# Performance work log

Hardware: AMD Instinct MI355X
Metric: run time of the kernel (lower is better)

## Reference

```python
import jax, jax.numpy as jnp
import numpy as np

D_MODEL, D_STATE, EXPAND = 256, 16, 2
D_INNER = EXPAND * D_MODEL
DT_RANK = (D_MODEL + 15) // 16
BATCH, SEQLEN = 4, 4096


def silu(x):
    return x * jax.nn.sigmoid(x)


def setup_inputs() -> dict:
    key = jax.random.key(0)
    ks = jax.random.split(key, 10)
    h = jax.random.normal(ks[0], (BATCH, SEQLEN, D_MODEL), dtype=jnp.float32)
    Wi_f = jax.random.normal(ks[1], (2 * D_INNER, D_MODEL), dtype=jnp.float32) / np.sqrt(D_MODEL)
    Wi_b = jax.random.normal(ks[2], (2 * D_INNER, D_MODEL), dtype=jnp.float32) / np.sqrt(D_MODEL)
    Wx_f = jax.random.normal(ks[3], (DT_RANK + 2 * D_STATE, D_INNER), dtype=jnp.float32) / np.sqrt(D_INNER)
    Wx_b = jax.random.normal(ks[4], (DT_RANK + 2 * D_STATE, D_INNER), dtype=jnp.float32) / np.sqrt(D_INNER)
    dt_std = DT_RANK ** -0.5
    Wdt_f = jax.random.uniform(ks[5], (D_INNER, DT_RANK), dtype=jnp.float32, minval=-dt_std, maxval=dt_std)
    Wdt_b = jax.random.uniform(ks[6], (D_INNER, DT_RANK), dtype=jnp.float32, minval=-dt_std, maxval=dt_std)
    # dt bias = inverse-softplus of dt sampled log-uniform in [1e-3, 1e-1]
    dt = jnp.exp(jax.random.uniform(ks[7], (D_INNER,), dtype=jnp.float32) * (np.log(0.1) - np.log(0.001)) + np.log(0.001))
    dt = jnp.clip(dt, 1e-4, None)
    inv_dt = dt + jnp.log(-jnp.expm1(-dt))
    bdt_f = inv_dt
    bdt_b = inv_dt
    A_log = jnp.log(jnp.broadcast_to(jnp.arange(1, D_STATE + 1, dtype=jnp.float32), (D_INNER, D_STATE)))
    A_log_f = A_log
    A_log_b = A_log
    D_f = jnp.ones((D_INNER,), dtype=jnp.float32)
    D_b = jnp.ones((D_INNER,), dtype=jnp.float32)
    Wo = jax.random.normal(ks[8], (D_MODEL, 2 * D_INNER), dtype=jnp.float32) / np.sqrt(2 * D_INNER)
    return {"hidden_states": h, "Wi_f": Wi_f, "Wi_b": Wi_b, "Wx_f": Wx_f, "Wx_b": Wx_b,
            "Wdt_f": Wdt_f, "Wdt_b": Wdt_b, "bdt_f": bdt_f, "bdt_b": bdt_b,
            "A_log_f": A_log_f, "A_log_b": A_log_b, "D_f": D_f, "D_b": D_b, "Wo": Wo}


def mamba_dir(h, Wi, Wx, Wdt, bdt, A_log, Dp, reverse):
    b, l, _ = h.shape
    di, r = Wdt.shape
    n = A_log.shape[1]
    xz = h @ Wi.T                      # [b,l,2*di]
    if reverse:
        xz = xz[:, ::-1]
    x, z = xz[..., :di], xz[..., di:]
    u = silu(x)                        # selective_scan input u
    x_dbl = u @ Wx.T                   # [b,l,r+2n]
    delta = jax.nn.softplus(x_dbl[..., :r] @ Wdt.T + bdt)   # [b,l,di]
    Bm = x_dbl[..., r:r + n]           # [b,l,n]
    Cm = x_dbl[..., r + n:r + 2 * n]   # [b,l,n]
    A = -jnp.exp(A_log)                # [di,n]

    def step(s, inp):
        u_t, d_t, B_t, C_t = inp       # [b,di],[b,di],[b,n],[b,n]
        dA = jnp.exp(d_t[..., None] * A)                         # [b,di,n]
        s = dA * s + (d_t * u_t)[..., None] * B_t[:, None, :]    # [b,di,n]
        y_t = jnp.einsum('bdn,bn->bd', s, C_t)
        return s, y_t

    s0 = jnp.zeros((b, di, n), dtype=u.dtype)
    xs = (jnp.swapaxes(u, 0, 1), jnp.swapaxes(delta, 0, 1),
          jnp.swapaxes(Bm, 0, 1), jnp.swapaxes(Cm, 0, 1))
    _, ys = jax.lax.scan(step, s0, xs)
    y = jnp.swapaxes(ys, 0, 1) + u * Dp          # skip term D*u
    y = y * silu(z)                              # gated output
    if reverse:
        y = y[:, ::-1]
    return y


def reference(hidden_states, Wi_f, Wi_b, Wx_f, Wx_b, Wdt_f, Wdt_b, bdt_f, bdt_b, A_log_f, A_log_b, D_f, D_b, Wo):
    y_f = mamba_dir(hidden_states, Wi_f, Wx_f, Wdt_f, bdt_f, A_log_f, D_f, False)
    y_b = mamba_dir(hidden_states, Wi_b, Wx_b, Wdt_b, bdt_b, A_log_b, D_b, True)
    y = jnp.concatenate([y_f, y_b], axis=-1)     # [b,l,2*di]
    return y @ Wo.T                              # [b,l,d_model]
```

## Files before the change

kernel.cpp:

```cpp
#include <hip/hip_runtime.h>
#include <hip/hip_bf16.h>
#include <cstddef>
#include <cstdint>

#define D_MODELc 256
#define D_STATEc 16
#define D_INNERc 512
#define DT_RANKc 16
#define BATCHc   4
#define SEQLENc  4096
#define NCHUNK   128
#define CHUNK    32

typedef unsigned short u16;
typedef __attribute__((ext_vector_type(8))) short bf16x8;
typedef __attribute__((ext_vector_type(4))) float f32x4;

__device__ __forceinline__ float siluf(float v) { return v / (1.f + __expf(-v)); }

__device__ __forceinline__ u16 bf16_rne(float f) {
    uint32_t u = __float_as_uint(f);
    u += 0x7fffu + ((u >> 16) & 1u);
    return (u16)(u >> 16);
}
__device__ __forceinline__ float bf16_to_f(u16 h) {
    return __uint_as_float(((uint32_t)h) << 16);
}
__device__ __forceinline__ float softplusf(float x) {
    return fmaxf(x, 0.f) + __logf(1.f + __expf(-fabsf(x)));
}

#define GLL16(g, l) __builtin_amdgcn_global_load_lds( \
    (const __attribute__((address_space(1))) uint32_t*)(g), \
    (__attribute__((address_space(3))) uint32_t*)(l), 16, 0, 0)

__global__ __launch_bounds__(256) void split_kernel(const float* __restrict__ in,
                                                    u16* __restrict__ hi,
                                                    u16* __restrict__ lo, int n4) {
    int i = blockIdx.x * 256 + threadIdx.x;
    const int stride = gridDim.x * 256;
    for (; i < n4; i += stride) {
        float4 v = ((const float4*)in)[i];
        u16 h0 = bf16_rne(v.x), h1 = bf16_rne(v.y), h2 = bf16_rne(v.z), h3 = bf16_rne(v.w);
        ushort4 hv; hv.x = h0; hv.y = h1; hv.z = h2; hv.w = h3;
        ushort4 lv;
        lv.x = bf16_rne(v.x - bf16_to_f(h0));
        lv.y = bf16_rne(v.y - bf16_to_f(h1));
        lv.z = bf16_rne(v.z - bf16_to_f(h2));
        lv.w = bf16_rne(v.w - bf16_to_f(h3));
        ((ushort4*)hi)[i] = hv;
        ((ushort4*)lo)[i] = lv;
    }
}

template<int EPI, int NBL2>
__global__ __launch_bounds__(256) void gemm_mfma(
        const u16* __restrict__ Ah, const u16* __restrict__ Al, int lda,
        const u16* __restrict__ Bh, const u16* __restrict__ Bl, int ldb,
        float* __restrict__ out0,
        u16* __restrict__ uh, u16* __restrict__ ul,
        int M, int N, int K) {
    __shared__ u16 lds[2][4][4][128][8];
    const int t    = threadIdx.x;
    const int lane = t & 63;
    const int wid  = t >> 6;
    const int wrow = wid >> 1, wcol = wid & 1;

    const int id  = blockIdx.x;
    const int xcd = id & 7;
    const int j   = id >> 3;
    const int nb  = j & ((1 << NBL2) - 1);
    const int mg  = j >> NBL2;
    const int m0  = (mg * 8 + xcd) * 128;
    const int n0  = nb * 128;

    const int lr  = lane & 15;
    const int kgl = lane >> 4;

    f32x4 acc[4][4] = {};

    auto stage = [&](int buf, int k0) {
        #pragma unroll
        for (int i = 0; i < 8; i++) {
            int c    = i * 256 + t;
            int tile = c >> 9;
            int kg   = (c >> 7) & 3;
            int row  = c & 127;
            const u16* bsrc = (tile == 0) ? Ah : (tile == 1) ? Al : (tile == 2) ? Bh : Bl;
            int r0 = (tile < 2) ? m0 : n0;
            int ld = (tile < 2) ? lda : ldb;
            const u16* g = bsrc + (size_t)(r0 + row) * ld + k0 + kg * 8;
            GLL16(g, ((char*)lds) + (size_t)buf * 32768 + (size_t)c * 16);
        }
    };

    const int NT = K >> 5;
    stage(0, 0);
    __syncthreads();

    for (int kt = 0; kt < NT; ++kt) {
        const int buf = kt & 1;
        if (kt + 1 < NT) stage(buf ^ 1, (kt + 1) * 32);

        bf16x8 afh[4], afl[4];
        #pragma unroll
        for (int mi = 0; mi < 4; mi++) {
            afh[mi] = *(const bf16x8*)&lds[buf][0][kgl][wrow * 64 + mi * 16 + lr][0];
            afl[mi] = *(const bf16x8*)&lds[buf][1][kgl][wrow * 64 + mi * 16 + lr][0];
        }
        #pragma unroll
        for (int ni = 0; ni < 4; ni++) {
            bf16x8 bfh = *(const bf16x8*)&lds[buf][2][kgl][wcol * 64 + ni * 16 + lr][0];
            bf16x8 bfl = *(const bf16x8*)&lds[buf][3][kgl][wcol * 64 + ni * 16 + lr][0];
            #pragma unroll
            for (int mi = 0; mi < 4; mi++) {
                acc[mi][ni] = __builtin_amdgcn_mfma_f32_16x16x32_bf16(afh[mi], bfh, acc[mi][ni], 0, 0, 0);
                acc[mi][ni] = __builtin_amdgcn_mfma_f32_16x16x32_bf16(afh[mi], bfl, acc[mi][ni], 0, 0, 0);
                acc[mi][ni] = __builtin_amdgcn_mfma_f32_16x16x32_bf16(afl[mi], bfh, acc[mi][ni], 0, 0, 0);
            }
        }
        __syncthreads();
    }

    #pragma unroll
    for (int mi = 0; mi < 4; mi++) {
        #pragma unroll
        for (int ni = 0; ni < 4; ni++) {
            #pragma unroll
            for (int r = 0; r < 4; r++) {
                int m = m0 + wrow * 64 + mi * 16 + kgl * 4 + r;
                int n = n0 + wcol * 64 + ni * 16 + lr;
                float v = acc[mi][ni][r];
                if (EPI == 0) {
                    out0[(size_t)m * N + n] = v;
                } else {
                    float s = siluf(v);
                    int dirn = n >> 10;
                    int nn   = n & 1023;
                    size_t dof = (size_t)dirn * (size_t)M * 512;
                    if (nn < 512) {
                        size_t idx = dof + (size_t)m * 512 + nn;
                        u16 sh = bf16_rne(s);
                        uh[idx] = sh;
                        ul[idx] = bf16_rne(s - bf16_to_f(sh));
                    } else {
                        out0[dof + (size_t)m * 512 + (nn - 512)] = s;
                    }
                }
            }
        }
    }
}

__global__ __launch_bounds__(256) void xdbl_mfma(
        const u16* __restrict__ Uh, const u16* __restrict__ Ul,
        const u16* __restrict__ WxH, const u16* __restrict__ WxL,
        float* __restrict__ out) {
    __shared__ u16 lds[2][4][64][8];
    const int t    = threadIdx.x;
    const int lane = t & 63;
    const int wid  = t >> 6;
    const int m0   = blockIdx.x * 64;
    const int dir  = blockIdx.y;
    const int Mp   = gridDim.x * 64;
    const int lr   = lane & 15;
    const int kgl  = lane >> 4;

    const size_t dofU = (size_t)dir * (size_t)Mp * 512;
    const size_t dofW = (size_t)dir * (size_t)48 * 512;
    const u16* Ah = Uh + dofU;
    const u16* Al = Ul + dofU;

    f32x4 acc[3] = {};

    for (int k0 = 0; k0 < 512; k0 += 32) {
        #pragma unroll
        for (int i = 0; i < 2; i++) {
            int c    = i * 256 + t;
            int tile = c >> 8;
            int kg   = (c >> 6) & 3;
            int row  = c & 63;
            const u16* bsrc = tile ? Al : Ah;
            const u16* g = bsrc + (size_t)(m0 + row) * 512 + k0 + kg * 8;
            GLL16(g, ((char*)lds) + (size_t)c * 16);
        }
        __syncthreads();

        bf16x8 afh = *(const bf16x8*)&lds[0][kgl][wid * 16 + lr][0];
        bf16x8 afl = *(const bf16x8*)&lds[1][kgl][wid * 16 + lr][0];
        #pragma unroll
        for (int nf = 0; nf < 3; nf++) {
            const size_t boff = dofW + (size_t)(nf * 16 + lr) * 512 + k0 + kgl * 8;
            bf16x8 bfh = *(const bf16x8*)(WxH + boff);
            bf16x8 bfl = *(const bf16x8*)(WxL + boff);
            acc[nf] = __builtin_amdgcn_mfma_f32_16x16x32_bf16(afh, bfh, acc[nf], 0, 0, 0);
            acc[nf] = __builtin_amdgcn_mfma_f32_16x16x32_bf16(afh, bfl, acc[nf], 0, 0, 0);
            acc[nf] = __builtin_amdgcn_mfma_f32_16x16x32_bf16(afl, bfh, acc[nf], 0, 0, 0);
        }
        __syncthreads();
    }

    float* o = out + (size_t)dir * (size_t)Mp * 48;
    #pragma unroll
    for (int nf = 0; nf < 3; nf++) {
        #pragma unroll
        for (int r = 0; r < 4; r++) {
            int m = m0 + wid * 16 + kgl * 4 + r;
            int n = nf * 16 + lr;
            o[(size_t)m * 48 + n] = acc[nf][r];
        }
    }
}

__global__ __launch_bounds__(256) void scan_phaseA(
        const u16* __restrict__ Uh, const u16* __restrict__ Ul,
        const float* __restrict__ XD,
        const float* __restrict__ Wdt_f, const float* __restrict__ Wdt_b,
        const float* __restrict__ bdt_f, const float* __restrict__ bdt_b,
        const float* __restrict__ AL_f, const float* __restrict__ AL_b,
        float* __restrict__ SDL, float* __restrict__ S) {
    const int c   = blockIdx.x;
    const int d   = blockIdx.y * 256 + threadIdx.x;
    const int z   = blockIdx.z;
    const int dir = z & 1;
    const int b   = z >> 1;
    const int PB  = gridDim.z >> 1;
    const int Mp  = PB * SEQLENc;
    const float* Wdt = dir ? Wdt_b : Wdt_f;
    const float* bdt = dir ? bdt_b : bdt_f;
    const float* AL  = dir ? AL_b  : AL_f;
    const u16* UhD = Uh + (size_t)dir * Mp * 512;
    const u16* UlD = Ul + (size_t)dir * Mp * 512;
    const float* XDD = XD + (size_t)dir * Mp * 48;

    float w[16], a[16], s[16];
    #pragma unroll
    for (int n = 0; n < 16; n++) {
        w[n] = Wdt[d * 16 + n];
        a[n] = -__expf(AL[d * 16 + n]);
        s[n] = 0.f;
    }
    const float a0 = a[0];
    bool pw = (a0 != 0.f);
    #pragma unroll
    for (int n = 1; n < 16; n++)
        pw = pw && (fabsf(a[n] - (float)(n + 1) * a0) <= 3e-6f * fabsf(a[n]));
    const float bb = bdt[d];
    float sdl = 0.f;

    for (int i = 0; i < CHUNK; i++) {
        int tt = c * CHUNK + i;
        int l  = dir ? (SEQLENc - 1 - tt) : tt;
        size_t row = (size_t)b * SEQLENc + l;
        float uu = bf16_to_f(UhD[row * 512 + d]) + bf16_to_f(UlD[row * 512 + d]);
        const float4* xr4 = (const float4*)&XDD[row * 48];
        float acc = bb;
        #pragma unroll
        for (int k = 0; k < 4; k++) {
            float4 xa = xr4[k];
            acc += xa.x*w[k*4+0] + xa.y*w[k*4+1] + xa.z*w[k*4+2] + xa.w*w[k*4+3];
        }
        float dl = softplusf(acc);
        sdl += dl;
        float du = dl * uu;
        if (pw) {
            float q = __expf(a0 * dl);
            float dAn = 1.f;
            #pragma unroll
            for (int g = 0; g < 4; g++) {
                float4 B4 = xr4[4 + g];
                float bx[4] = {B4.x, B4.y, B4.z, B4.w};
                #pragma unroll
                for (int jj = 0; jj < 4; jj++) {
                    int n = g * 4 + jj;
                    dAn *= q;
                    s[n] = dAn * s[n] + du * bx[jj];
                }
            }
        } else {
            #pragma unroll
            for (int g = 0; g < 4; g++) {
                float4 B4 = xr4[4 + g];
                float bx[4] = {B4.x, B4.y, B4.z, B4.w};
                #pragma unroll
                for (int jj = 0; jj < 4; jj++) {
                    int n = g * 4 + jj;
                    float dA = __expf(dl * a[n]);
                    s[n] = dA * s[n] + du * bx[jj];
                }
            }
        }
    }
    SDL[((size_t)z * NCHUNK + c) * 512 + d] = sdl;
    size_t base = (((size_t)z * NCHUNK + c) * 16) * 512 + d;
    #pragma unroll
    for (int n = 0; n < 16; n++)
        S[base + (size_t)n * 512] = s[n];
}

__global__ __launch_bounds__(256) void scan_phaseB(const float* __restrict__ SDL,
                                                   float* __restrict__ S,
                                                   const float* __restrict__ AL_f,
                                                   const float* __restrict__ AL_b) {
    const int g   = blockIdx.x * 256 + threadIdx.x;
    const int d   = g & 511;
    const int n   = (g >> 9) & 15;
    const int z   = g >> 13;
    const int dir = z & 1;
    const float an = -__expf((dir ? AL_b : AL_f)[d * 16 + n]);
    const size_t strideS = (size_t)16 * 512;
    size_t offS = (((size_t)z * NCHUNK) * 16 + n) * 512 + d;
    size_t offD = ((size_t)z * NCHUNK) * 512 + d;
    float carry = 0.f;
    float sdl = SDL[offD], ss = S[offS];
    for (int c = 0; c < NCHUNK; c++) {
        float sdn = 0.f, sn = 0.f;
        if (c + 1 < NCHUNK) { sdn = SDL[offD + 512]; sn = S[offS + strideS]; }
        float pp = __expf(an * sdl);
        S[offS] = carry;
        carry = pp * carry + ss;
        sdl = sdn; ss = sn;
        offS += strideS; offD += 512;
    }
}

__global__ __launch_bounds__(256) void scan_phaseC(
        const u16* __restrict__ Uh, const u16* __restrict__ Ul,
        const float* __restrict__ XD,
        const float* __restrict__ Wdt_f, const float* __restrict__ Wdt_b,
        const float* __restrict__ bdt_f, const float* __restrict__ bdt_b,
        const float* __restrict__ AL_f, const float* __restrict__ AL_b,
        const float* __restrict__ E,
        const float* __restrict__ SZ,
        const float* __restrict__ D_f,  const float* __restrict__ D_b,
        u16* __restrict__ Yh, u16* __restrict__ Yl) {
    const int c   = blockIdx.x;
    const int d   = blockIdx.y * 256 + threadIdx.x;
    const int z   = blockIdx.z;
    const int dir = z & 1;
    const int b   = z >> 1;
    const int PB  = gridDim.z >> 1;
    const int Mp  = PB * SEQLENc;
    const float* Wdt = dir ? Wdt_b : Wdt_f;
    const float* bdt = dir ? bdt_b : bdt_f;
    const float* AL  = dir ? AL_b  : AL_f;
    const u16* UhD = Uh + (size_t)dir * Mp * 512;
    const u16* UlD = Ul + (size_t)dir * Mp * 512;
    const float* XDD = XD + (size_t)dir * Mp * 48;
    const float* SZD = SZ + (size_t)dir * Mp * 512;

    float w[16], a[16], s[16];
    size_t base = (((size_t)z * NCHUNK + c) * 16) * 512 + d;
    #pragma unroll
    for (int n = 0; n < 16; n++) {
        w[n] = Wdt[d * 16 + n];
        a[n] = -__expf(AL[d * 16 + n]);
        s[n] = E[base + (size_t)n * 512];
    }
    const float a0 = a[0];
    bool pw = (a0 != 0.f);
    #pragma unroll
    for (int n = 1; n < 16; n++)
        pw = pw && (fabsf(a[n] - (float)(n + 1) * a0) <= 3e-6f * fabsf(a[n]));
    const float bb = bdt[d];
    const float Dd = (dir ? D_b : D_f)[d];

    for (int i = 0; i < CHUNK; i++) {
        int tt = c * CHUNK + i;
        int l  = dir ? (SEQLENc - 1 - tt) : tt;
        size_t row = (size_t)b * SEQLENc + l;
        float uu = bf16_to_f(UhD[row * 512 + d]) + bf16_to_f(UlD[row * 512 + d]);
        const float4* xr4 = (const float4*)&XDD[row * 48];
        float acc = bb;
        #pragma unroll
        for (int k = 0; k < 4; k++) {
            float4 xa = xr4[k];
            acc += xa.x*w[k*4+0] + xa.y*w[k*4+1] + xa.z*w[k*4+2] + xa.w*w[k*4+3];
        }
        float dl = softplusf(acc);
        float du = dl * uu;
        float y = 0.f;
        if (pw) {
            float q = __expf(a0 * dl);
            float dAn = 1.f;
            #pragma unroll
            for (int g = 0; g < 4; g++) {
                float4 B4 = xr4[4 + g];
                float4 C4 = xr4[8 + g];
                float bx[4] = {B4.x, B4.y, B4.z, B4.w};
                float cx[4] = {C4.x, C4.y, C4.z, C4.w};
                #pragma unroll
                for (int jj = 0; jj < 4; jj++) {
                    int n = g * 4 + jj;
                    dAn *= q;
                    s[n] = dAn * s[n] + du * bx[jj];
                    y += s[n] * cx[jj];
                }
            }
        } else {
            #pragma unroll
            for (int g = 0; g < 4; g++) {
                float4 B4 = xr4[4 + g];
                float4 C4 = xr4[8 + g];
                float bx[4] = {B4.x, B4.y, B4.z, B4.w};
                float cx[4] = {C4.x, C4.y, C4.z, C4.w};
                #pragma unroll
                for (int jj = 0; jj < 4; jj++) {
                    int n = g * 4 + jj;
                    float dA = __expf(dl * a[n]);
                    s[n] = dA * s[n] + du * bx[jj];
                    y += s[n] * cx[jj];
                }
            }
        }
        float yv = (y + uu * Dd) * SZD[row * 512 + d];
        size_t yi = row * 1024 + (size_t)dir * 512 + d;
        u16 yh = bf16_rne(yv);
        Yh[yi] = yh;
        Yl[yi] = bf16_rne(yv - bf16_to_f(yh));
    }
}

extern "C" void kernel_launch(void* const* d_in, const int* in_sizes, int n_in,
                              void* d_out, int out_size, void* d_ws, size_t ws_size,
                              hipStream_t stream) {
    const float* h    = (const float*)d_in[0];
    const float* Wi_f = (const float*)d_in[1];
    const float* Wi_b = (const float*)d_in[2];
    const float* Wx_f = (const float*)d_in[3];
    const float* Wx_b = (const float*)d_in[4];
    const float* Wdt_f= (const float*)d_in[5];
    const float* Wdt_b= (const float*)d_in[6];
    const float* bdt_f= (const float*)d_in[7];
    const float* bdt_b= (const float*)d_in[8];
    const float* Al_f = (const float*)d_in[9];
    const float* Al_b = (const float*)d_in[10];
    const float* D_f  = (const float*)d_in[11];
    const float* D_b  = (const float*)d_in[12];
    const float* Wo   = (const float*)d_in[13];
    float* out = (float*)d_out;

    const size_t W_ELE  = 1024 * 256;
    const size_t WX_ELE = 48 * 512;
    const size_t FB   = (size_t)SEQLENc * D_INNERc;
    const size_t FH   = (size_t)SEQLENc * D_MODELc;
    const size_t FX   = (size_t)SEQLENc * 48;
    const size_t FP   = (size_t)NCHUNK * 16 * 512;
    const size_t FD   = (size_t)NCHUNK * 512;
    const size_t FY   = (size_t)SEQLENc * 1024;

    const size_t fixed_bytes = (8 * W_ELE + 4 * WX_ELE) * sizeof(u16);
    const size_t per_b = 2 * FH * sizeof(u16)
                       + 2 * FB * sizeof(float)
                       + 4 * FB * sizeof(u16)
                       + 2 * FX * sizeof(float)
                       + 2 * (FP + FD) * sizeof(float)
                       + 2 * FY * sizeof(u16);
    int PB = 4;
    if (fixed_bytes + 4 * per_b + 65536 > ws_size) PB = 2;
    if (fixed_bytes + 2 * per_b + 65536 > ws_size) PB = 1;

    char* cur = (char*)d_ws;
    auto alloc = [&](size_t bytes) -> char* {
        char* p = cur; cur += (bytes + 255) & ~(size_t)255; return p;
    };
    u16* WiH = (u16*)alloc(2 * W_ELE * 2);
    u16* WiL = (u16*)alloc(2 * W_ELE * 2);
    u16* WoH = (u16*)alloc(W_ELE * 2);
    u16* WoL = (u16*)alloc(W_ELE * 2);
    u16* WxH = (u16*)alloc(2 * WX_ELE * 2);
    u16* WxL = (u16*)alloc(2 * WX_ELE * 2);
    u16*   hH = (u16*)alloc((size_t)PB * FH * 2);
    u16*   hL = (u16*)alloc((size_t)PB * FH * 2);
    float* sz = (float*)alloc((size_t)PB * 2 * FB * 4);
    u16*   uhB= (u16*)alloc((size_t)PB * 2 * FB * 2);
    u16*   ulB= (u16*)alloc((size_t)PB * 2 * FB * 2);
    float* xd = (float*)alloc((size_t)PB * 2 * FX * 4);
    float* SDL= (float*)alloc((size_t)PB * 2 * FD * 4);
    float* S  = (float*)alloc((size_t)PB * 2 * FP * 4);
    u16*   yH = (u16*)alloc((size_t)PB * FY * 2);
    u16*   yL = (u16*)alloc((size_t)PB * FY * 2);

    {
        int n4 = (int)(W_ELE / 4);
        int blocks = (n4 + 255) / 256; if (blocks > 1024) blocks = 1024;
        split_kernel<<<blocks, 256, 0, stream>>>(Wi_f, WiH, WiL, n4);
        split_kernel<<<blocks, 256, 0, stream>>>(Wi_b, WiH + W_ELE, WiL + W_ELE, n4);
        split_kernel<<<blocks, 256, 0, stream>>>(Wo,   WoH, WoL, n4);
        int nx4 = (int)(WX_ELE / 4);
        split_kernel<<<(nx4 + 255) / 256, 256, 0, stream>>>(Wx_f, WxH, WxL, nx4);
        split_kernel<<<(nx4 + 255) / 256, 256, 0, stream>>>(Wx_b, WxH + WX_ELE, WxL + WX_ELE, nx4);
    }

    for (int b0 = 0; b0 < BATCHc; b0 += PB) {
        const int Mp = PB * SEQLENc;
        const int MB = Mp / 128;
        const float* hB = h   + (size_t)b0 * FH;
        float*       oB = out + (size_t)b0 * FH;

        {
            int n4 = (int)((size_t)PB * FH / 4);
            int blocks = (n4 + 255) / 256; if (blocks > 2048) blocks = 2048;
            split_kernel<<<blocks, 256, 0, stream>>>(hB, hH, hL, n4);
        }

        gemm_mfma<1, 4><<<16 * MB, 256, 0, stream>>>(
            hH, hL, D_MODELc, WiH, WiL, D_MODELc,
            sz, uhB, ulB, Mp, 2048, D_MODELc);

        xdbl_mfma<<<dim3(Mp / 64, 2), 256, 0, stream>>>(uhB, ulB, WxH, WxL, xd);

        scan_phaseA<<<dim3(NCHUNK, 2, 2 * PB), 256, 0, stream>>>(
            uhB, ulB, xd, Wdt_f, Wdt_b, bdt_f, bdt_b, Al_f, Al_b, SDL, S);
        scan_phaseB<<<PB * 64, 256, 0, stream>>>(SDL, S, Al_f, Al_b);
        scan_phaseC<<<dim3(NCHUNK, 2, 2 * PB), 256, 0, stream>>>(
            uhB, ulB, xd, Wdt_f, Wdt_b, bdt_f, bdt_b, Al_f, Al_b,
            S, sz, D_f, D_b, yH, yL);

        gemm_mfma<0, 1><<<2 * MB, 256, 0, stream>>>(
            yH, yL, 1024, WoH, WoL, 1024,
            oB, nullptr, nullptr, Mp, D_MODELc, 1024);
    }
}
```

Baseline: 371.6 us.

## Interleave hi/lo bf16 split pairs into packed 32-bit words and use nontemporal accesses

Stores the hi/lo bf16 split of u and y as one packed 32-bit word per element instead of two separate u16 arrays. The scan kernels then read a single 4-byte word per element, and the GEMM and xdbl kernels unpack fragments from LDS with a new interleaved staging path. Most global loads and stores also become nontemporal hints, aiming to cut separate scattered 2-byte transactions and cache pollution. The cost is extra ALU work to unpack fragments, and the nontemporal hints may hurt when data is reused through the cache.

Result: slower. 416.9 us (+12.2%).

```diff
diff --git a/kernel.cpp b/kernel.cpp
--- a/kernel.cpp
+++ b/kernel.cpp
@@ -15,6 +15,7 @@
 typedef unsigned short u16;
 typedef __attribute__((ext_vector_type(8))) short bf16x8;
 typedef __attribute__((ext_vector_type(4))) float f32x4;
+typedef float __attribute__((ext_vector_type(4))) f4v;
 
 __device__ __forceinline__ float siluf(float v) { return v / (1.f + __expf(-v)); }
 
@@ -25,6 +26,24 @@
 }
 __device__ __forceinline__ float bf16_to_f(u16 h) {
     return __uint_as_float(((uint32_t)h) << 16);
+}
+__device__ __forceinline__ uint32_t pack_hl(float f) {
+    u16 hh = bf16_rne(f);
+    u16 ll = bf16_rne(f - bf16_to_f(hh));
+    return ((uint32_t)hh << 16) | ll;
+}
+__device__ __forceinline__ float unpack_add(uint32_t v) {
+    return __uint_as_float(v & 0xFFFF0000u) + __uint_as_float(v << 16);
+}
+__device__ __forceinline__ void unpack_frag(const uint32_t* q, bf16x8& fh, bf16x8& fl) {
+    union { bf16x8 v; uint32_t w[4]; } H, L;
+    #pragma unroll
+    for (int i = 0; i < 4; i++) {
+        uint32_t a = q[2 * i], b = q[2 * i + 1];
+        H.w[i] = (a >> 16) | (b & 0xFFFF0000u);
+        L.w[i] = (a & 0xFFFFu) | (b << 16);
+    }
+    fh = H.v; fl = L.v;
 }
 __device__ __forceinline__ float softplusf(float x) {
     return fmaxf(x, 0.f) + __logf(1.f + __expf(-fabsf(x)));
@@ -53,14 +72,14 @@
     }
 }
 
-template<int EPI, int NBL2>
+template<int EPI, int NBL2, int AINT>
 __global__ __launch_bounds__(256) void gemm_mfma(
         const u16* __restrict__ Ah, const u16* __restrict__ Al, int lda,
         const u16* __restrict__ Bh, const u16* __restrict__ Bl, int ldb,
         float* __restrict__ out0,
-        u16* __restrict__ uh, u16* __restrict__ ul,
+        uint32_t* __restrict__ uhl,
         int M, int N, int K) {
-    __shared__ u16 lds[2][4][4][128][8];
+    __shared__ char lds[2][32768];
     const int t    = threadIdx.x;
     const int lane = t & 63;
     const int wid  = t >> 6;
@@ -80,17 +99,40 @@
     f32x4 acc[4][4] = {};
 
     auto stage = [&](int buf, int k0) {
-        #pragma unroll
-        for (int i = 0; i < 8; i++) {
-            int c    = i * 256 + t;
-            int tile = c >> 9;
-            int kg   = (c >> 7) & 3;
-            int row  = c & 127;
-            const u16* bsrc = (tile == 0) ? Ah : (tile == 1) ? Al : (tile == 2) ? Bh : Bl;
-            int r0 = (tile < 2) ? m0 : n0;
-            int ld = (tile < 2) ? lda : ldb;
-            const u16* g = bsrc + (size_t)(r0 + row) * ld + k0 + kg * 8;
-            GLL16(g, ((char*)lds) + (size_t)buf * 32768 + (size_t)c * 16);
+        if (AINT == 0) {
+            #pragma unroll
+            for (int i = 0; i < 8; i++) {
+                int c    = i * 256 + t;
+                int tile = c >> 9;
+                int kg   = (c >> 7) & 3;
+                int row  = c & 127;
+                const u16* bsrc = (tile == 0) ? Ah : (tile == 1) ? Al : (tile == 2) ? Bh : Bl;
+                int r0 = (tile < 2) ? m0 : n0;
+                int ld = (tile < 2) ? lda : ldb;
+                const u16* g = bsrc + (size_t)(r0 + row) * ld + k0 + kg * 8;
+                GLL16(g, &lds[buf][c * 16]);
+            }
+        } else {
+            const uint32_t* Aint = (const uint32_t*)Ah;
+            #pragma unroll
+            for (int i = 0; i < 8; i++) {
+                int c = i * 256 + t;
+                if (c < 1024) {
+                    int kg   = c >> 8;
+                    int row  = (c >> 1) & 127;
+                    int half = c & 1;
+                    const uint32_t* g = Aint + (size_t)(m0 + row) * lda + k0 + kg * 8 + half * 4;
+                    GLL16(g, &lds[buf][c * 16]);
+                } else {
+                    int cb   = c - 1024;
+                    int tile = cb >> 9;
+                    int kg   = (cb >> 7) & 3;
+                    int row  = cb & 127;
+                    const u16* bsrc = tile ? Bl : Bh;
+                    const u16* g = bsrc + (size_t)(n0 + row) * ldb + k0 + kg * 8;
+                    GLL16(g, &lds[buf][c * 16]);
+                }
+            }
         }
     };
 
@@ -103,15 +145,28 @@
         if (kt + 1 < NT) stage(buf ^ 1, (kt + 1) * 32);
 
         bf16x8 afh[4], afl[4];
-        #pragma unroll
-        for (int mi = 0; mi < 4; mi++) {
-            afh[mi] = *(const bf16x8*)&lds[buf][0][kgl][wrow * 64 + mi * 16 + lr][0];
-            afl[mi] = *(const bf16x8*)&lds[buf][1][kgl][wrow * 64 + mi * 16 + lr][0];
-        }
+        if (AINT == 0) {
+            const u16* lb = (const u16*)lds[buf];
+            #pragma unroll
+            for (int mi = 0; mi < 4; mi++) {
+                int row = wrow * 64 + mi * 16 + lr;
+                afh[mi] = *(const bf16x8*)(lb + 0 * 4096 + kgl * 1024 + row * 8);
+                afl[mi] = *(const bf16x8*)(lb + 1 * 4096 + kgl * 1024 + row * 8);
+            }
+        } else {
+            const uint32_t* la = (const uint32_t*)lds[buf];
+            #pragma unroll
+            for (int mi = 0; mi < 4; mi++) {
+                int row = wrow * 64 + mi * 16 + lr;
+                unpack_frag(la + kgl * 1024 + row * 8, afh[mi], afl[mi]);
+            }
+        }
+        const u16* lbB = (const u16*)(lds[buf] + (AINT ? 16384 : 16384));
         #pragma unroll
         for (int ni = 0; ni < 4; ni++) {
-            bf16x8 bfh = *(const bf16x8*)&lds[buf][2][kgl][wcol * 64 + ni * 16 + lr][0];
-            bf16x8 bfl = *(const bf16x8*)&lds[buf][3][kgl][wcol * 64 + ni * 16 + lr][0];
+            int row = wcol * 64 + ni * 16 + lr;
+            bf16x8 bfh = *(const bf16x8*)(lbB + 0 * 4096 + kgl * 1024 + row * 8);
+            bf16x8 bfl = *(const bf16x8*)(lbB + 1 * 4096 + kgl * 1024 + row * 8);
             #pragma unroll
             for (int mi = 0; mi < 4; mi++) {
                 acc[mi][ni] = __builtin_amdgcn_mfma_f32_16x16x32_bf16(afh[mi], bfh, acc[mi][ni], 0, 0, 0);
@@ -132,19 +187,16 @@
                 int n = n0 + wcol * 64 + ni * 16 + lr;
                 float v = acc[mi][ni][r];
                 if (EPI == 0) {
-                    out0[(size_t)m * N + n] = v;
+                    __builtin_nontemporal_store(v, &out0[(size_t)m * N + n]);
                 } else {
                     float s = siluf(v);
                     int dirn = n >> 10;
                     int nn   = n & 1023;
                     size_t dof = (size_t)dirn * (size_t)M * 512;
                     if (nn < 512) {
-                        size_t idx = dof + (size_t)m * 512 + nn;
-                        u16 sh = bf16_rne(s);
-                        uh[idx] = sh;
-                        ul[idx] = bf16_rne(s - bf16_to_f(sh));
+                        __builtin_nontemporal_store(pack_hl(s), &uhl[dof + (size_t)m * 512 + nn]);
                     } else {
-                        out0[dof + (size_t)m * 512 + (nn - 512)] = s;
+                        __builtin_nontemporal_store(s, &out0[dof + (size_t)m * 512 + (nn - 512)]);
                     }
                 }
             }
@@ -153,10 +205,10 @@
 }
 
 __global__ __launch_bounds__(256) void xdbl_mfma(
-        const u16* __restrict__ Uh, const u16* __restrict__ Ul,
+        const uint32_t* __restrict__ Uhl,
         const u16* __restrict__ WxH, const u16* __restrict__ WxL,
         float* __restrict__ out) {
-    __shared__ u16 lds[2][4][64][8];
+    __shared__ uint32_t lds[4][64][8];
     const int t    = threadIdx.x;
     const int lane = t & 63;
     const int wid  = t >> 6;
@@ -168,8 +220,6 @@
 
     const size_t dofU = (size_t)dir * (size_t)Mp * 512;
     const size_t dofW = (size_t)dir * (size_t)48 * 512;
-    const u16* Ah = Uh + dofU;
-    const u16* Al = Ul + dofU;
 
     f32x4 acc[3] = {};
 
@@ -177,17 +227,16 @@
         #pragma unroll
         for (int i = 0; i < 2; i++) {
             int c    = i * 256 + t;
-            int tile = c >> 8;
-            int kg   = (c >> 6) & 3;
-            int row  = c & 63;
-            const u16* bsrc = tile ? Al : Ah;
-            const u16* g = bsrc + (size_t)(m0 + row) * 512 + k0 + kg * 8;
+            int kg   = c >> 7;
+            int row  = (c >> 1) & 63;
+            int half = c & 1;
+            const uint32_t* g = Uhl + dofU + (size_t)(m0 + row) * 512 + k0 + kg * 8 + half * 4;
             GLL16(g, ((char*)lds) + (size_t)c * 16);
         }
         __syncthreads();
 
-        bf16x8 afh = *(const bf16x8*)&lds[0][kgl][wid * 16 + lr][0];
-        bf16x8 afl = *(const bf16x8*)&lds[1][kgl][wid * 16 + lr][0];
+        bf16x8 afh, afl;
+        unpack_frag(&lds[kgl][wid * 16 + lr][0], afh, afl);
         #pragma unroll
         for (int nf = 0; nf < 3; nf++) {
             const size_t boff = dofW + (size_t)(nf * 16 + lr) * 512 + k0 + kgl * 8;
@@ -207,13 +256,13 @@
         for (int r = 0; r < 4; r++) {
             int m = m0 + wid * 16 + kgl * 4 + r;
             int n = nf * 16 + lr;
-            o[(size_t)m * 48 + n] = acc[nf][r];
+            __builtin_nontemporal_store(acc[nf][r], &o[(size_t)m * 48 + n]);
         }
     }
 }
 
 __global__ __launch_bounds__(256) void scan_phaseA(
-        const u16* __restrict__ Uh, const u16* __restrict__ Ul,
+        const uint32_t* __restrict__ Uhl,
         const float* __restrict__ XD,
         const float* __restrict__ Wdt_f, const float* __restrict__ Wdt_b,
         const float* __restrict__ bdt_f, const float* __restrict__ bdt_b,
@@ -229,8 +278,7 @@
     const float* Wdt = dir ? Wdt_b : Wdt_f;
     const float* bdt = dir ? bdt_b : bdt_f;
     const float* AL  = dir ? AL_b  : AL_f;
-    const u16* UhD = Uh + (size_t)dir * Mp * 512;
-    const u16* UlD = Ul + (size_t)dir * Mp * 512;
+    const uint32_t* UD = Uhl + (size_t)dir * Mp * 512;
     const float* XDD = XD + (size_t)dir * Mp * 48;
 
     float w[16], a[16], s[16];
@@ -252,13 +300,13 @@
         int tt = c * CHUNK + i;
         int l  = dir ? (SEQLENc - 1 - tt) : tt;
         size_t row = (size_t)b * SEQLENc + l;
-        float uu = bf16_to_f(UhD[row * 512 + d]) + bf16_to_f(UlD[row * 512 + d]);
-        const float4* xr4 = (const float4*)&XDD[row * 48];
+        float uu = unpack_add(__builtin_nontemporal_load(&UD[row * 512 + d]));
+        const f4v* xr4 = (const f4v*)&XDD[row * 48];
         float acc = bb;
         #pragma unroll
         for (int k = 0; k < 4; k++) {
-            float4 xa = xr4[k];
-            acc += xa.x*w[k*4+0] + xa.y*w[k*4+1] + xa.z*w[k*4+2] + xa.w*w[k*4+3];
+            f4v xa = __builtin_nontemporal_load(xr4 + k);
+            acc += xa[0]*w[k*4+0] + xa[1]*w[k*4+1] + xa[2]*w[k*4+2] + xa[3]*w[k*4+3];
         }
         float dl = softplusf(acc);
         sdl += dl;
@@ -268,34 +316,32 @@
             float dAn = 1.f;
             #pragma unroll
             for (int g = 0; g < 4; g++) {
-                float4 B4 = xr4[4 + g];
-                float bx[4] = {B4.x, B4.y, B4.z, B4.w};
+                f4v B4 = __builtin_nontemporal_load(xr4 + 4 + g);
                 #pragma unroll
                 for (int jj = 0; jj < 4; jj++) {
                     int n = g * 4 + jj;
                     dAn *= q;
-                    s[n] = dAn * s[n] + du * bx[jj];
+                    s[n] = dAn * s[n] + du * B4[jj];
                 }
             }
         } else {
             #pragma unroll
             for (int g = 0; g < 4; g++) {
-                float4 B4 = xr4[4 + g];
-                float bx[4] = {B4.x, B4.y, B4.z, B4.w};
+                f4v B4 = __builtin_nontemporal_load(xr4 + 4 + g);
                 #pragma unroll
                 for (int jj = 0; jj < 4; jj++) {
                     int n = g * 4 + jj;
                     float dA = __expf(dl * a[n]);
-                    s[n] = dA * s[n] + du * bx[jj];
+                    s[n] = dA * s[n] + du * B4[jj];
                 }
             }
         }
     }
-    SDL[((size_t)z * NCHUNK + c) * 512 + d] = sdl;
+    __builtin_nontemporal_store(sdl, &SDL[((size_t)z * NCHUNK + c) * 512 + d]);
     size_t base = (((size_t)z * NCHUNK + c) * 16) * 512 + d;
     #pragma unroll
     for (int n = 0; n < 16; n++)
-        S[base + (size_t)n * 512] = s[n];
+        __builtin_nontemporal_store(s[n], &S[base + (size_t)n * 512]);
 }
 
 __global__ __launch_bounds__(256) void scan_phaseB(const float* __restrict__ SDL,
@@ -317,7 +363,7 @@
         float sdn = 0.f, sn = 0.f;
         if (c + 1 < NCHUNK) { sdn = SDL[offD + 512]; sn = S[offS + strideS]; }
         float pp = __expf(an * sdl);
-        S[offS] = carry;
+        __builtin_nontemporal_store(carry, &S[offS]);
         carry = pp * carry + ss;
         sdl = sdn; ss = sn;
         offS += strideS; offD += 512;
@@ -325,7 +371,7 @@
 }
 
 __global__ __launch_bounds__(256) void scan_phaseC(
-        const u16* __restrict__ Uh, const u16* __restrict__ Ul,
+        const uint32_t* __restrict__ Uhl,
         const float* __restrict__ XD,
         const float* __restrict__ Wdt_f, const float* __restrict__ Wdt_b,
         const float* __restrict__ bdt_f, const float* __restrict__ bdt_b,
@@ -333,7 +379,7 @@
         const float* __restrict__ E,
         const float* __restrict__ SZ,
         const float* __restrict__ D_f,  const float* __restrict__ D_b,
-        u16* __restrict__ Yh, u16* __restrict__ Yl) {
+        uint32_t* __restrict__ Yhl) {
     const int c   = blockIdx.x;
     const int d   = blockIdx.y * 256 + threadIdx.x;
     const int z   = blockIdx.z;
@@ -344,8 +390,7 @@
     const float* Wdt = dir ? Wdt_b : Wdt_f;
     const float* bdt = dir ? bdt_b : bdt_f;
     const float* AL  = dir ? AL_b  : AL_f;
-    const u16* UhD = Uh + (size_t)dir * Mp * 512;
-    const u16* UlD = Ul + (size_t)dir * Mp * 512;
+    const uint32_t* UD = Uhl + (size_t)dir * Mp * 512;
     const float* XDD = XD + (size_t)dir * Mp * 48;
     const float* SZD = SZ + (size_t)dir * Mp * 512;
 
@@ -355,7 +400,7 @@
     for (int n = 0; n < 16; n++) {
         w[n] = Wdt[d * 16 + n];
         a[n] = -__expf(AL[d * 16 + n]);
-        s[n] = E[base + (size_t)n * 512];
+        s[n] = __builtin_nontemporal_load(&E[base + (size_t)n * 512]);
     }
     const float a0 = a[0];
     bool pw = (a0 != 0.f);
@@ -369,13 +414,13 @@
         int tt = c * CHUNK + i;
         int l  = dir ? (SEQLENc - 1 - tt) : tt;
         size_t row = (size_t)b * SEQLENc + l;
-        float uu = bf16_to_f(UhD[row * 512 + d]) + bf16_to_f(UlD[row * 512 + d]);
-        const float4* xr4 = (const float4*)&XDD[row * 48];
+        float uu = unpack_add(__builtin_nontemporal_load(&UD[row * 512 + d]));
+        const f4v* xr4 = (const f4v*)&XDD[row * 48];
         float acc = bb;
         #pragma unroll
         for (int k = 0; k < 4; k++) {
-            float4 xa = xr4[k];
-            acc += xa.x*w[k*4+0] + xa.y*w[k*4+1] + xa.z*w[k*4+2] + xa.w*w[k*4+3];
+            f4v xa = __builtin_nontemporal_load(xr4 + k);
+            acc += xa[0]*w[k*4+0] + xa[1]*w[k*4+1] + xa[2]*w[k*4+2] + xa[3]*w[k*4+3];
         }
         float dl = softplusf(acc);
         float du = dl * uu;
@@ -385,39 +430,33 @@
             float dAn = 1.f;
             #pragma unroll
             for (int g = 0; g < 4; g++) {
-                float4 B4 = xr4[4 + g];
-                float4 C4 = xr4[8 + g];
-                float bx[4] = {B4.x, B4.y, B4.z, B4.w};
-                float cx[4] = {C4.x, C4.y, C4.z, C4.w};
+                f4v B4 = __builtin_nontemporal_load(xr4 + 4 + g);
+                f4v C4 = __builtin_nontemporal_load(xr4 + 8 + g);
                 #pragma unroll
                 for (int jj = 0; jj < 4; jj++) {
                     int n = g * 4 + jj;
                     dAn *= q;
-                    s[n] = dAn * s[n] + du * bx[jj];
-                    y += s[n] * cx[jj];
+                    s[n] = dAn * s[n] + du * B4[jj];
+                    y += s[n] * C4[jj];
                 }
             }
         } else {
             #pragma unroll
             for (int g = 0; g < 4; g++) {
-                float4 B4 = xr4[4 + g];
-                float4 C4 = xr4[8 + g];
-                float bx[4] = {B4.x, B4.y, B4.z, B4.w};
-                float cx[4] = {C4.x, C4.y, C4.z, C4.w};
+                f4v B4 = __builtin_nontemporal_load(xr4 + 4 + g);
+                f4v C4 = __builtin_nontemporal_load(xr4 + 8 + g);
                 #pragma unroll
                 for (int jj = 0; jj < 4; jj++) {
                     int n = g * 4 + jj;
                     float dA = __expf(dl * a[n]);
-                    s[n] = dA * s[n] + du * bx[jj];
-                    y += s[n] * cx[jj];
+                    s[n] = dA * s[n] + du * B4[jj];
+                    y += s[n] * C4[jj];
                 }
             }
         }
-        float yv = (y + uu * Dd) * SZD[row * 512 + d];
-        size_t yi = row * 1024 + (size_t)dir * 512 + d;
-        u16 yh = bf16_rne(yv);
-        Yh[yi] = yh;
-        Yl[yi] = bf16_rne(yv - bf16_to_f(yh));
+        float sz = __builtin_nontemporal_load(&SZD[row * 512 + d]);
+        float yv = (y + uu * Dd) * sz;
+        __builtin_nontemporal_store(pack_hl(yv), &Yhl[row * 1024 + (size_t)dir * 512 + d]);
     }
 }
 
@@ -452,10 +491,10 @@
     const size_t fixed_bytes = (8 * W_ELE + 4 * WX_ELE) * sizeof(u16);
     const size_t per_b = 2 * FH * sizeof(u16)
                        + 2 * FB * sizeof(float)
-                       + 4 * FB * sizeof(u16)
+                       + 2 * FB * sizeof(uint32_t)
                        + 2 * FX * sizeof(float)
                        + 2 * (FP + FD) * sizeof(float)
-                       + 2 * FY * sizeof(u16);
+                       + FY * sizeof(uint32_t);
     int PB = 4;
     if (fixed_bytes + 4 * per_b + 65536 > ws_size) PB = 2;
     if (fixed_bytes + 2 * per_b + 65536 > ws_size) PB = 1;
@@ -470,16 +509,14 @@
     u16* WoL = (u16*)alloc(W_ELE * 2);
     u16* WxH = (u16*)alloc(2 * WX_ELE * 2);
     u16* WxL = (u16*)alloc(2 * WX_ELE * 2);
-    u16*   hH = (u16*)alloc((size_t)PB * FH * 2);
-    u16*   hL = (u16*)alloc((size_t)PB * FH * 2);
-    float* sz = (float*)alloc((size_t)PB * 2 * FB * 4);
-    u16*   uhB= (u16*)alloc((size_t)PB * 2 * FB * 2);
-    u16*   ulB= (u16*)alloc((size_t)PB * 2 * FB * 2);
-    float* xd = (float*)alloc((size_t)PB * 2 * FX * 4);
-    float* SDL= (float*)alloc((size_t)PB * 2 * FD * 4);
-    float* S  = (float*)alloc((size_t)PB * 2 * FP * 4);
-    u16*   yH = (u16*)alloc((size_t)PB * FY * 2);
-    u16*   yL = (u16*)alloc((size_t)PB * FY * 2);
+    u16*      hH  = (u16*)alloc((size_t)PB * FH * 2);
+    u16*      hL  = (u16*)alloc((size_t)PB * FH * 2);
+    float*    sz  = (float*)alloc((size_t)PB * 2 * FB * 4);
+    uint32_t* uhl = (uint32_t*)alloc((size_t)PB * 2 * FB * 4);
+    float*    xd  = (float*)alloc((size_t)PB * 2 * FX * 4);
+    float*    SDL = (float*)alloc((size_t)PB * 2 * FD * 4);
+    float*    S   = (float*)alloc((size_t)PB * 2 * FP * 4);
+    uint32_t* yhl = (uint32_t*)alloc((size_t)PB * FY * 4);
 
     {
         int n4 = (int)(W_ELE / 4);
@@ -504,21 +541,21 @@
             split_kernel<<<blocks, 256, 0, stream>>>(hB, hH, hL, n4);
         }
 
-        gemm_mfma<1, 4><<<16 * MB, 256, 0, stream>>>(
+        gemm_mfma<1, 4, 0><<<16 * MB, 256, 0, stream>>>(
             hH, hL, D_MODELc, WiH, WiL, D_MODELc,
-            sz, uhB, ulB, Mp, 2048, D_MODELc);
-
-        xdbl_mfma<<<dim3(Mp / 64, 2), 256, 0, stream>>>(uhB, ulB, WxH, WxL, xd);
+            sz, uhl, Mp, 2048, D_MODELc);
+
+        xdbl_mfma<<<dim3(Mp / 64, 2), 256, 0, stream>>>(uhl, WxH, WxL, xd);
 
         scan_phaseA<<<dim3(NCHUNK, 2, 2 * PB), 256, 0, stream>>>(
-            uhB, ulB, xd, Wdt_f, Wdt_b, bdt_f, bdt_b, Al_f, Al_b, SDL, S);
+            uhl, xd, Wdt_f, Wdt_b, bdt_f, bdt_b, Al_f, Al_b, SDL, S);
         scan_phaseB<<<PB * 64, 256, 0, stream>>>(SDL, S, Al_f, Al_b);
         scan_phaseC<<<dim3(NCHUNK, 2, 2 * PB), 256, 0, stream>>>(
-            uhB, ulB, xd, Wdt_f, Wdt_b, bdt_f, bdt_b, Al_f, Al_b,
-            S, sz, D_f, D_b, yH, yL);
-
-        gemm_mfma<0, 1><<<2 * MB, 256, 0, stream>>>(
-            yH, yL, 1024, WoH, WoL, 1024,
-            oB, nullptr, nullptr, Mp, D_MODELc, 1024);
-    }
-}
+            uhl, xd, Wdt_f, Wdt_b, bdt_f, bdt_b, Al_f, Al_b,
+            S, sz, D_f, D_b, yhl);
+
+        gemm_mfma<0, 1, 1><<<2 * MB, 256, 0, stream>>>(
+            (const u16*)yhl, nullptr, 1024, WoH, WoL, 1024,
+            oB, nullptr, Mp, D_MODELc, 1024);
+    }
+}
```
